# Kernel tuning notes

Hardware: AMD Instinct MI355X
Metric: run time of the kernel (lower is better)

## Reference

```python
import jax, jax.numpy as jnp
import numpy as np
import math

B, T = 512, 512
ENC = 512          # 2 * input_size
N_MELS, R = 80, 2
ATTN, DEC = 256, 256
PRE_H, PRE_O = 256, 256
HID = 128          # DCA hidden
SC, SK = 8, 21     # static channels / kernel
DC, DK = 8, 21     # dynamic channels / kernel
PL, PA, PB = 11, 0.1, 0.9  # prior length, alpha, beta


def _betabinom_pmf(k, n, a, b):
    lg = math.lgamma
    return math.exp(lg(n + 1) - lg(k + 1) - lg(n - k + 1)
                    + lg(k + a) + lg(n - k + b) - lg(n + a + b)
                    - (lg(a) + lg(b) - lg(a + b)))


def setup_inputs() -> dict:
    key = jax.random.key(0)
    ks = iter(jax.random.split(key, 64))
    def rn(shape, s=0.05):
        return jax.random.normal(next(ks), shape, dtype=jnp.float32) * s
    inp = {}
    inp["h"] = rn([B, T, ENC], 1.0)
    inp["y"] = rn([B, N_MELS], 1.0)
    a = jax.random.uniform(next(ks), [B, T], dtype=jnp.float32)
    inp["alpha"] = a / a.sum(-1, keepdims=True)  # valid attention distribution
    inp["c"] = rn([B, ENC], 1.0)
    for n in ["attn_h0", "attn_c0", "rnn1_h0", "rnn1_c0", "rnn2_h0", "rnn2_c0"]:
        inp[n] = rn([B, ATTN], 1.0)
    # prenet
    inp["fc1_w"] = rn([PRE_H, N_MELS]); inp["fc1_b"] = rn([PRE_H])
    inp["fc2_w"] = rn([PRE_O, PRE_H]); inp["fc2_b"] = rn([PRE_O])
    # dynamic convolution attention
    inp["W_w"] = rn([HID, ATTN]); inp["W_b"] = rn([HID])
    inp["V_w"] = rn([DC * DK, HID])
    inp["F_w"] = rn([SC, 1, SK])
    inp["U_w"] = rn([HID, SC])
    inp["T_w"] = rn([HID, DC]); inp["T_b"] = rn([HID])
    inp["v_w"] = rn([1, HID])
    P = np.array([_betabinom_pmf(k, PL - 1, PA, PB) for k in range(PL)], np.float32)[::-1].copy()
    inp["P"] = jnp.asarray(P)
    # attn LSTM cell: input = 2*input_size + prenet output = 768
    inp["attn_wih"] = rn([4 * ATTN, ENC + PRE_O]); inp["attn_whh"] = rn([4 * ATTN, ATTN])
    inp["attn_bih"] = rn([4 * ATTN]); inp["attn_bhh"] = rn([4 * ATTN])
    inp["lin_w"] = rn([DEC, ENC + ATTN]); inp["lin_b"] = rn([DEC])
    for pfx in ["r1", "r2"]:
        inp[pfx + "_wih"] = rn([4 * DEC, DEC]); inp[pfx + "_whh"] = rn([4 * DEC, DEC])
        inp[pfx + "_bih"] = rn([4 * DEC]); inp[pfx + "_bhh"] = rn([4 * DEC])
    inp["proj_w"] = rn([N_MELS * R, DEC])
    return inp


def _lstm(x, h, c, wih, whh, bih, bhh):
    g = x @ wih.T + bih + h @ whh.T + bhh
    i, f, gg, o = jnp.split(g, 4, axis=-1)
    c2 = jax.nn.sigmoid(f) * c + jax.nn.sigmoid(i) * jnp.tanh(gg)
    return jax.nn.sigmoid(o) * jnp.tanh(c2), c2


def _win(x, k):
    # x: [B, T + k - 1] padded signal -> sliding windows [B, T, k]
    idx = jnp.arange(T)[:, None] + jnp.arange(k)[None, :]
    return x[:, idx]


def reference(h, y, alpha, c, attn_h0, attn_c0, rnn1_h0, rnn1_c0, rnn2_h0, rnn2_c0,
              fc1_w, fc1_b, fc2_w, fc2_b, W_w, W_b, V_w, F_w, U_w, T_w, T_b, v_w, P,
              attn_wih, attn_whh, attn_bih, attn_bhh, lin_w, lin_b,
              r1_wih, r1_whh, r1_bih, r1_bhh, r2_wih, r2_whh, r2_bih, r2_bhh, proj_w):
    # prenet (eval mode -> dropout inactive since fixed=False)
    yp = jax.nn.relu(jax.nn.relu(y @ fc1_w.T + fc1_b) @ fc2_w.T + fc2_b)
    attn_h, attn_c = _lstm(jnp.concatenate([c, yp], -1), attn_h0, attn_c0,
                           attn_wih, attn_whh, attn_bih, attn_bhh)
    # --- dynamic convolution attention ---
    # prior: causal conv with flipped beta-binomial pmf
    p = jnp.einsum('btk,k->bt', _win(jnp.pad(alpha, ((0, 0), (PL - 1, 0))), PL), P)
    p = jnp.log(jnp.clip(p, 1e-6))
    # dynamic filters per batch element: [B, DC, DK]
    G = (jnp.tanh(attn_h @ W_w.T + W_b) @ V_w.T).reshape(-1, DC, DK)
    wd = _win(jnp.pad(alpha, ((0, 0), ((DK - 1) // 2, (DK - 1) // 2))), DK)  # [B,T,DK]
    g = jnp.einsum('btk,bck->btc', wd, G)  # grouped conv1d, groups=B
    ws = _win(jnp.pad(alpha, ((0, 0), ((SK - 1) // 2, (SK - 1) // 2))), SK)
    f = jnp.einsum('btk,ck->btc', ws, F_w[:, 0, :])  # static conv1d
    e = jnp.squeeze(jnp.tanh(f @ U_w.T + g @ T_w.T + T_b) @ v_w.T, -1) + p
    alpha2 = jax.nn.softmax(e, axis=-1)
    # --- context + decoder stack ---
    c2 = jnp.einsum('bt,btd->bd', alpha2, h)
    x = jnp.concatenate([c2, attn_h], -1) @ lin_w.T + lin_b
    r1_h, r1_c = _lstm(x, rnn1_h0, rnn1_c0, r1_wih, r1_whh, r1_bih, r1_bhh)
    x = x + r1_h
    r2_h, r2_c = _lstm(x, rnn2_h0, rnn2_c0, r2_wih, r2_whh, r2_bih, r2_bhh)
    x = x + r2_h
    out = (x @ proj_w.T).reshape(-1, N_MELS, R)
    return (out, alpha2, c2, attn_h, attn_c, r1_h, r1_c, r2_h, r2_c)
```

## Files before the change

### kernel.cpp

```cpp
#include <hip/hip_runtime.h>

typedef unsigned short u16;

__device__ __forceinline__ float bf2f(u16 u) { return __uint_as_float(((unsigned)u) << 16); }
__device__ __forceinline__ float ldraw(const void* p, size_t i, int dt) {
    return dt ? ((const float*)p)[i] : bf2f(((const u16*)p)[i]);
}
__device__ __forceinline__ int fl(const int* F, int f) { return f < 0 ? 1 : F[f]; }
__device__ __forceinline__ float fast_tanh(float x) {
    x = fminf(fmaxf(x, -15.f), 15.f);
    float e = __expf(2.f * x);
    return (e - 1.f) / (e + 1.f);
}
__device__ __forceinline__ float sigm(float x) { return 1.f / (1.f + __expf(-x)); }

__global__ __launch_bounds__(256) void k_detect(int* __restrict__ flagsRaw,
    const void* p0, const void* p1, const void* p2, const void* p3, const void* p4,
    const void* p5, const void* p6, const void* p7, const void* p8, const void* p9,
    const void* p10, const void* p11, const void* p12, const void* p13, const void* p14,
    const void* p15, const void* p16, const void* p17, const void* p18, const void* p19,
    const void* p20, const void* p21, const void* p22, const void* p23, const void* p24,
    const void* p25, const void* p26, const void* p27, const void* p28, const void* p29,
    const void* p30, const void* p31, const void* p32, const void* p33, const void* p34,
    const void* p35, const void* p36, const void* p37)
{
    const void* ptrs[38] = {p0,p1,p2,p3,p4,p5,p6,p7,p8,p9,p10,p11,p12,p13,p14,p15,p16,
                            p17,p18,p19,p20,p21,p22,p23,p24,p25,p26,p27,p28,p29,p30,p31,
                            p32,p33,p34,p35,p36,p37};
    const int ns[38] = {134217728, 40960, 262144, 262144,
                        131072,131072,131072,131072,131072,131072,
                        20480,256,65536,256,
                        32768,128,21504,168,1024,1024,128,128,11,
                        786432,262144,1024,1024, 196608,256,
                        262144,262144,1024,1024, 262144,262144,1024,1024, 40960};
    __shared__ int s;
    int b = blockIdx.x, tid = threadIdx.x;
    if (tid == 0) s = 0;
    __syncthreads();
    int nsamp = ns[b] >> 1;
    if (nsamp > 512) nsamp = 512;
    const u16* q = (const u16*)ptrs[b];
    int bad = 0;
    for (int i = tid; i < nsamp; i += 256) {
        u16 u = q[2 * i];
        int e = (u >> 7) & 0xff;
        bad += (e < 96 || e > 159) ? 1 : 0;
    }
    atomicAdd(&s, bad);
    __syncthreads();
    if (tid == 0) flagsRaw[b] = (s * 4 > nsamp) ? 1 : 0;
}

__global__ __launch_bounds__(256) void k_finish(
    const int* __restrict__ FRAW, int* __restrict__ FF,
    const void* U_w, const void* T_w, const void* T_b, const void* v_w, const void* F_w,
    float* utw, float* tbf, float* vf, float* ff)
{
    __shared__ int sflag[38];
    const int big[38] = {1,1,1,1, 1,1,1,1,1,1, 1,0,1,0,
                         1,0,1,0,1,1,0,0,0, 1,1,1,1, 1,0,
                         1,1,1,1, 1,1,1,1, 1};
    int tid = threadIdx.x;
    if (tid == 0) {
        int s = 0, c = 0;
        for (int i = 0; i < 38; i++) if (big[i]) { s += FRAW[i]; c++; }
        int maj = (s * 2 > c) ? 1 : 0;
        for (int i = 0; i < 38; i++) { int v = big[i] ? FRAW[i] : maj; sflag[i] = v; FF[i] = v; }
    }
    __syncthreads();
    int dU = sflag[18], dT = sflag[19], dTb = sflag[20], dV = sflag[21], dF = sflag[17];
    for (int i = tid; i < 1024; i += 256) {
        int j = i >> 3, c = i & 7;
        utw[j * 16 + c]     = ldraw(U_w, i, dU);
        utw[j * 16 + 8 + c] = ldraw(T_w, i, dT);
    }
    if (tid < 128) { tbf[tid] = ldraw(T_b, tid, dTb); vf[tid] = ldraw(v_w, tid, dV); }
    if (tid < 168) ff[tid] = ldraw(F_w, tid, dF);
}

__device__ __forceinline__ void vg32_pair(const int* F,
    const void* A, int lda, int fa, const void* B, int ldb, int bo, int fb, int K,
    int m0, int n0, int N, int tid, int tx, int ty, float* acc,
    float As[32][68], float Bs[32][68])
{
    int dA = fl(F, fa), dB = fl(F, fb);
    bool fastp = dA && dB;
    for (int k0 = 0; k0 < K; k0 += 64) {
        __syncthreads();
        if (fastp) {
            #pragma unroll
            for (int p = 0; p < 2; p++) {
                int e = tid + p * 256;
                int row = e >> 4, kk = (e & 15) * 4;
                float4 va = {0.f, 0.f, 0.f, 0.f};
                if (k0 + kk < K)
                    va = *(const float4*)((const float*)A + (size_t)(m0 + row) * lda + k0 + kk);
                *(float4*)&As[row][kk] = va;
                int nr = n0 + row;
                float4 vb = {0.f, 0.f, 0.f, 0.f};
                if (nr < N && k0 + kk < K)
                    vb = *(const float4*)((const float*)B + (size_t)nr * ldb + bo + k0 + kk);
                *(float4*)&Bs[row][kk] = vb;
            }
        } else {
            #pragma unroll
            for (int p = 0; p < 8; p++) {
                int e = tid + p * 256;
                int row = e >> 6, kk = e & 63;
                As[row][kk] = (k0 + kk < K) ? ldraw(A, (size_t)(m0 + row) * lda + k0 + kk, dA) : 0.f;
                int nr = n0 + row;
                Bs[row][kk] = (nr < N && k0 + kk < K)
                            ? ldraw(B, (size_t)nr * ldb + bo + k0 + kk, dB) : 0.f;
            }
        }
        __syncthreads();
        #pragma unroll
        for (int kq = 0; kq < 16; kq++) {
            float4 a0 = *(const float4*)&As[ty][kq * 4];
            float4 a1 = *(const float4*)&As[ty + 16][kq * 4];
            float4 b0 = *(const float4*)&Bs[tx][kq * 4];
            float4 b1 = *(const float4*)&Bs[tx + 16][kq * 4];
            acc[0] += a0.x*b0.x + a0.y*b0.y + a0.z*b0.z + a0.w*b0.w;
            acc[1] += a0.x*b1.x + a0.y*b1.y + a0.z*b1.z + a0.w*b1.w;
            acc[2] += a1.x*b0.x + a1.y*b0.y + a1.z*b0.z + a1.w*b0.w;
            acc[3] += a1.x*b1.x + a1.y*b1.y + a1.z*b1.z + a1.w*b1.w;
        }
    }
}

__global__ __launch_bounds__(256) void k_vgemm32(
    const int* __restrict__ F,
    const void* A1, int lda1, int fa1, const void* B1, int ldb1, int bo1, int fb1, int K1,
    const void* A2, int lda2, int fa2, const void* B2, int ldb2, int bo2, int fb2, int K2,
    const void* A3, int lda3, int fa3, const void* B3, int ldb3, int bo3, int fb3, int K3,
    const void* bias1, int fx1, const void* bias2, int fx2,
    float* __restrict__ Cf, int ldc, int N, int act)
{
    __shared__ float As[32][68], Bs[32][68];
    int tid = threadIdx.x, tx = tid & 15, ty = tid >> 4;
    int m0 = blockIdx.y * 32, n0 = blockIdx.x * 32;
    float acc[4] = {0.f, 0.f, 0.f, 0.f};
    vg32_pair(F, A1, lda1, fa1, B1, ldb1, bo1, fb1, K1, m0, n0, N, tid, tx, ty, acc, As, Bs);
    if (A2) vg32_pair(F, A2, lda2, fa2, B2, ldb2, bo2, fb2, K2, m0, n0, N, tid, tx, ty, acc, As, Bs);
    if (A3) vg32_pair(F, A3, lda3, fa3, B3, ldb3, bo3, fb3, K3, m0, n0, N, tid, tx, ty, acc, As, Bs);

    #pragma unroll
    for (int c = 0; c < 2; c++) {
        int n = n0 + tx + c * 16;
        if (n >= N) continue;
        float bias = 0.f;
        if (bias1) bias += ldraw(bias1, n, fl(F, fx1));
        if (bias2) bias += ldraw(bias2, n, fl(F, fx2));
        #pragma unroll
        for (int r = 0; r < 2; r++) {
            float v = acc[r * 2 + c] + bias;
            if (act == 1) v = fmaxf(v, 0.f);
            else if (act == 2) v = fast_tanh(v);
            Cf[(size_t)(m0 + ty + r * 16) * ldc + n] = v;
        }
    }
}

__device__ __forceinline__ void lstm_pair(const int* F,
    const void* A, int lda, int fa, const void* B, int ldb, int bo, int fb, int K,
    int b0, int j0, int tid, int tx, int ty, float* acc,
    float As[16][68], float Bs[64][68])
{
    int dA = fl(F, fa), dB = fl(F, fb);
    bool fastp = dA && dB;
    for (int k0 = 0; k0 < K; k0 += 64) {
        __syncthreads();
        if (fastp) {
            {
                int e = tid;
                int row = e >> 4, kk = (e & 15) * 4;
                float4 va = {0.f, 0.f, 0.f, 0.f};
                if (k0 + kk < K)
                    va = *(const float4*)((const float*)A + (size_t)(b0 + row) * lda + k0 + kk);
                *(float4*)&As[row][kk] = va;
            }
            #pragma unroll
            for (int p = 0; p < 4; p++) {
                int e = tid + p * 256;
                int brow = e >> 4, kk = (e & 15) * 4;
                int grow = (brow >> 4) * 256 + j0 + (brow & 15);
                float4 vb = {0.f, 0.f, 0.f, 0.f};
                if (k0 + kk < K)
                    vb = *(const float4*)((const float*)B + (size_t)grow * ldb + bo + k0 + kk);
                *(float4*)&Bs[brow][kk] = vb;
            }
        } else {
            #pragma unroll
            for (int p = 0; p < 4; p++) {
                int e = tid + p * 256;
                int row = e >> 6, kk = e & 63;
                As[row][kk] = (k0 + kk < K) ? ldraw(A, (size_t)(b0 + row) * lda + k0 + kk, dA) : 0.f;
            }
            #pragma unroll
            for (int p = 0; p < 16; p++) {
                int e = tid + p * 256;
                int brow = e >> 6, kk = e & 63;
                int grow = (brow >> 4) * 256 + j0 + (brow & 15);
                Bs[brow][kk] = (k0 + kk < K)
                             ? ldraw(B, (size_t)grow * ldb + bo + k0 + kk, dB) : 0.f;
            }
        }
        __syncthreads();
        #pragma unroll
        for (int kq = 0; kq < 16; kq++) {
            float4 a = *(const float4*)&As[ty][kq * 4];
            #pragma unroll
            for (int g = 0; g < 4; g++) {
                float4 b = *(const float4*)&Bs[g * 16 + tx][kq * 4];
                acc[g] += a.x*b.x + a.y*b.y + a.z*b.z + a.w*b.w;
            }
        }
    }
}

__global__ __launch_bounds__(256) void k_lstm(
    const int* __restrict__ F,
    const void* A1, int lda1, int fa1, const void* B1, int ldb1, int bo1, int fb1, int K1,
    const void* A2, int lda2, int fa2, const void* B2, int ldb2, int bo2, int fb2, int K2,
    const void* A3, int lda3, int fa3, const void* B3, int ldb3, int bo3, int fb3, int K3,
    const void* bih, int fx1, const void* bhh, int fx2,
    const void* c0, int fc0,
    float* __restrict__ h_out, float* __restrict__ c_out,
    const float* __restrict__ xprev, float* __restrict__ xout)
{
    __shared__ float As[16][68];
    __shared__ float Bs[64][68];
    int tid = threadIdx.x, tx = tid & 15, ty = tid >> 4;
    int j0 = blockIdx.x * 16, b0 = blockIdx.y * 16;
    float acc[4] = {0.f, 0.f, 0.f, 0.f};
    lstm_pair(F, A1, lda1, fa1, B1, ldb1, bo1, fb1, K1, b0, j0, tid, tx, ty, acc, As, Bs);
    if (A2) lstm_pair(F, A2, lda2, fa2, B2, ldb2, bo2, fb2, K2, b0, j0, tid, tx, ty, acc, As, Bs);
    if (A3) lstm_pair(F, A3, lda3, fa3, B3, ldb3, bo3, fb3, K3, b0, j0, tid, tx, ty, acc, As, Bs);

    int j = j0 + tx, b = b0 + ty;
    int dx1 = fl(F, fx1), dx2 = fl(F, fx2);
    float gi = acc[0] + ldraw(bih, j, dx1)       + ldraw(bhh, j, dx2);
    float gf = acc[1] + ldraw(bih, j + 256, dx1) + ldraw(bhh, j + 256, dx2);
    float gg = acc[2] + ldraw(bih, j + 512, dx1) + ldraw(bhh, j + 512, dx2);
    float go = acc[3] + ldraw(bih, j + 768, dx1) + ldraw(bhh, j + 768, dx2);
    size_t idx = (size_t)b * 256 + j;
    float cp = ldraw(c0, idx, F[fc0]);
    float cn = sigm(gf) * cp + sigm(gi) * fast_tanh(gg);
    float hn = sigm(go) * fast_tanh(cn);
    h_out[idx] = hn;
    c_out[idx] = cn;
    if (xprev) xout[idx] = xprev[idx] + hn;
}

__global__ __launch_bounds__(256) void k_dca(
    const int* __restrict__ F, const void* __restrict__ alpha, const void* __restrict__ P,
    const float* __restrict__ G, const float* __restrict__ utw, const float* __restrict__ tbf,
    const float* __restrict__ vf, const float* __restrict__ ff,
    float* __restrict__ o_a2)
{
    __shared__ float4 sut[512];
    __shared__ float stb[128], sv[128], sff[168], sgd[168], sal[532], spf[16], sred[8];
    int dA = F[2], dP = F[22];
    int b = blockIdx.x, tid = threadIdx.x;
    for (int i = tid; i < 512; i += 256) sut[i] = ((const float4*)utw)[i];
    if (tid < 128) { stb[tid] = tbf[tid]; sv[tid] = vf[tid]; }
    if (tid < 168) { sff[tid] = ff[tid]; sgd[tid] = G[(size_t)b * 168 + tid]; }
    if (tid < 11)  spf[tid] = ldraw(P, tid, dP);
    for (int i = tid; i < 532; i += 256)
        sal[i] = (i >= 10 && i < 522) ? ldraw(alpha, (size_t)b * 512 + i - 10, dA) : 0.f;
    __syncthreads();

    float e[2];
    #pragma unroll
    for (int q = 0; q < 2; q++) {
        int t = tid + q * 256;
        float aw[21];
        #pragma unroll
        for (int k = 0; k < 21; k++) aw[k] = sal[t + k];
        float pv = 0.f;
        #pragma unroll
        for (int k = 0; k < 11; k++) pv += aw[k] * spf[k];
        float fc[8], gc[8];
        #pragma unroll
        for (int c = 0; c < 8; c++) {
            float s1 = 0.f, s2 = 0.f;
            #pragma unroll
            for (int k = 0; k < 21; k++) {
                s1 += aw[k] * sff[c * 21 + k];
                s2 += aw[k] * sgd[c * 21 + k];
            }
            fc[c] = s1; gc[c] = s2;
        }
        float ev = 0.f;
        #pragma unroll 4
        for (int j = 0; j < 128; j++) {
            float4 u0 = sut[j * 4 + 0], u1 = sut[j * 4 + 1];
            float4 t0 = sut[j * 4 + 2], t1 = sut[j * 4 + 3];
            float a = stb[j];
            a += fc[0] * u0.x + fc[1] * u0.y + fc[2] * u0.z + fc[3] * u0.w;
            a += fc[4] * u1.x + fc[5] * u1.y + fc[6] * u1.z + fc[7] * u1.w;
            a += gc[0] * t0.x + gc[1] * t0.y + gc[2] * t0.z + gc[3] * t0.w;
            a += gc[4] * t1.x + gc[5] * t1.y + gc[6] * t1.z + gc[7] * t1.w;
            ev += fast_tanh(a) * sv[j];
        }
        e[q] = ev + __logf(fmaxf(pv, 1e-6f));
    }

    float m = fmaxf(e[0], e[1]);
    #pragma unroll
    for (int off = 32; off >= 1; off >>= 1) m = fmaxf(m, __shfl_xor(m, off));
    if ((tid & 63) == 0) sred[tid >> 6] = m;
    __syncthreads();
    m = fmaxf(fmaxf(sred[0], sred[1]), fmaxf(sred[2], sred[3]));
    float x0 = __expf(e[0] - m), x1 = __expf(e[1] - m);
    float s = x0 + x1;
    #pragma unroll
    for (int off = 32; off >= 1; off >>= 1) s += __shfl_xor(s, off);
    if ((tid & 63) == 0) sred[4 + (tid >> 6)] = s;
    __syncthreads();
    s = sred[4] + sred[5] + sred[6] + sred[7];
    float inv = 1.f / s;
    o_a2[(size_t)b * 512 + tid]       = x0 * inv;
    o_a2[(size_t)b * 512 + tid + 256] = x1 * inv;
}

__global__ __launch_bounds__(256) void k_c2_part(
    const int* __restrict__ F, const float* __restrict__ a2,
    const void* __restrict__ h, float* __restrict__ part)
{
    int dH = F[0];
    int bi = blockIdx.x;
    int b = bi >> 1, sp = bi & 1;
    int tid = threadIdx.x;
    int dsub = (tid & 63) * 8;
    int tsub = tid >> 6;
    __shared__ float sa[256];
    sa[tid] = a2[(size_t)b * 512 + sp * 256 + tid];
    __syncthreads();
    float acc[8];
    #pragma unroll
    for (int j = 0; j < 8; j++) acc[j] = 0.f;
    size_t rowbase = (size_t)b * 512 + sp * 256;
    if (dH) {
        const float* hf = (const float*)h;
        for (int tt = tsub; tt < 256; tt += 4) {
            float a = sa[tt];
            const float* p = hf + (rowbase + tt) * 512 + dsub;
            float4 v0 = *(const float4*)p, v1 = *(const float4*)(p + 4);
            acc[0] += a * v0.x; acc[1] += a * v0.y; acc[2] += a * v0.z; acc[3] += a * v0.w;
            acc[4] += a * v1.x; acc[5] += a * v1.y; acc[6] += a * v1.z; acc[7] += a * v1.w;
        }
    } else {
        const u16* hb = (const u16*)h;
        for (int tt = tsub; tt < 256; tt += 4) {
            float a = sa[tt];
            const u16* p = hb + (rowbase + tt) * 512 + dsub;
            #pragma unroll
            for (int j = 0; j < 8; j++) acc[j] += a * bf2f(p[j]);
        }
    }
    __shared__ float sacc[256 * 8];
    #pragma unroll
    for (int j = 0; j < 8; j++) sacc[tid * 8 + j] = acc[j];
    __syncthreads();
    if (tid < 64) {
        float* pp = part + ((size_t)sp * 512 + b) * 512 + tid * 8;
        #pragma unroll
        for (int j = 0; j < 8; j++)
            pp[j] = sacc[tid * 8 + j] + sacc[(tid + 64) * 8 + j]
                  + sacc[(tid + 128) * 8 + j] + sacc[(tid + 192) * 8 + j];
    }
}

__global__ void k_c2_red(const float* __restrict__ part, float* __restrict__ o_c2)
{
    int idx = blockIdx.x * 256 + threadIdx.x;
    o_c2[idx] = part[idx] + part[idx + 262144];
}

__global__ void k_plant_direct(float* out0, float v) {
    if (threadIdx.x == 0 && blockIdx.x == 0) out0[0] = v;
}

extern "C" void kernel_launch(void* const* d_in, const int* in_sizes, int n_in,
                              void* d_out, int out_size, void* d_ws, size_t ws_size,
                              hipStream_t stream)
{
    (void)out_size; (void)ws_size;
    float* outf = (float*)d_out;

    static const int exp_sizes[38] = {
        134217728, 40960, 262144, 262144,
        131072,131072,131072,131072,131072,131072,
        20480,256,65536,256,
        32768,128,21504,168,1024,1024,128,128,11,
        786432,262144,1024,1024, 196608,256,
        262144,262144,1024,1024, 262144,262144,1024,1024, 40960};
    int bad = 0;
    if (n_in != 38) bad = 100;
    else for (int i = 0; i < 38; i++)
        if (in_sizes[i] != exp_sizes[i]) { bad = i + 1; break; }
    if (bad) {
        k_plant_direct<<<1, 1, 0, stream>>>(outf, 4194304.f + 65536.f * (float)bad);
        return;
    }

    const void* h_enc  = d_in[0];  const void* y      = d_in[1];
    const void* alpha  = d_in[2];  const void* c_in   = d_in[3];
    const void* ah0    = d_in[4];  const void* ac0    = d_in[5];
    const void* r1h0   = d_in[6];  const void* r1c0   = d_in[7];
    const void* r2h0   = d_in[8];  const void* r2c0   = d_in[9];
    const void* fc1_w  = d_in[10]; const void* fc1_b  = d_in[11];
    const void* fc2_w  = d_in[12]; const void* fc2_b  = d_in[13];
    const void* W_w    = d_in[14]; const void* W_b    = d_in[15];
    const void* V_w    = d_in[16]; const void* F_w    = d_in[17];
    const void* U_w    = d_in[18]; const void* T_w    = d_in[19];
    const void* T_b    = d_in[20]; const void* v_w    = d_in[21];
    const void* P      = d_in[22];
    const void* a_wih  = d_in[23]; const void* a_whh  = d_in[24];
    const void* a_bih  = d_in[25]; const void* a_bhh  = d_in[26];
    const void* lin_w  = d_in[27]; const void* lin_b  = d_in[28];
    const void* r1_wih = d_in[29]; const void* r1_whh = d_in[30];
    const void* r1_bih = d_in[31]; const void* r1_bhh = d_in[32];
    const void* r2_wih = d_in[33]; const void* r2_whh = d_in[34];
    const void* r2_bih = d_in[35]; const void* r2_bhh = d_in[36];
    const void* proj_w = d_in[37];

    char* ws = (char*)d_ws;
    int*   FRAW = (int*)  (ws + 0);
    int*   FF   = (int*)  (ws + 256);
    float* utw  = (float*)(ws + 1024);
    float* tbf  = (float*)(ws + 9216);
    float* vf   = (float*)(ws + 9728);
    float* ffs  = (float*)(ws + 10240);
    float* h1f  = (float*)(ws + 12288);
    float* ypf  = (float*)(ws + 536576);
    float* thf  = (float*)(ws + 1060864);
    float* Gdf  = (float*)(ws + 1323008);
    float* part = (float*)(ws + 1667072);

    float* o_out = outf + 0;
    float* o_a2  = outf + 81920;
    float* o_c2  = outf + 344064;
    float* o_ah  = outf + 606208;
    float* o_ac  = outf + 737280;
    float* o_r1h = outf + 868352;
    float* o_r1c = outf + 999424;
    float* o_r2h = outf + 1130496;
    float* o_r2c = outf + 1261568;

    const void* nv = nullptr;
    dim3 blk(256, 1, 1);

    k_detect<<<38, blk, 0, stream>>>(FRAW,
        d_in[0], d_in[1], d_in[2], d_in[3], d_in[4], d_in[5], d_in[6], d_in[7], d_in[8],
        d_in[9], d_in[10], d_in[11], d_in[12], d_in[13], d_in[14], d_in[15], d_in[16],
        d_in[17], d_in[18], d_in[19], d_in[20], d_in[21], d_in[22], d_in[23], d_in[24],
        d_in[25], d_in[26], d_in[27], d_in[28], d_in[29], d_in[30], d_in[31], d_in[32],
        d_in[33], d_in[34], d_in[35], d_in[36], d_in[37]);
    k_finish<<<1, blk, 0, stream>>>(FRAW, FF, U_w, T_w, T_b, v_w, F_w, utw, tbf, vf, ffs);

    k_vgemm32<<<dim3(8, 16), blk, 0, stream>>>(FF,
        y, 80, 1, fc1_w, 80, 0, 10, 80,
        nv, 0, -1, nv, 0, 0, -1, 0,  nv, 0, -1, nv, 0, 0, -1, 0,
        fc1_b, 11, nv, -1, h1f, 256, 256, 1);
    k_vgemm32<<<dim3(8, 16), blk, 0, stream>>>(FF,
        h1f, 256, -1, fc2_w, 256, 0, 12, 256,
        nv, 0, -1, nv, 0, 0, -1, 0,  nv, 0, -1, nv, 0, 0, -1, 0,
        fc2_b, 13, nv, -1, ypf, 256, 256, 1);

    k_lstm<<<dim3(16, 32), blk, 0, stream>>>(FF,
        c_in, 512, 3, a_wih, 768, 0, 23, 512,
        ypf, 256, -1, a_wih, 768, 512, 23, 256,
        ah0, 256, 4, a_whh, 256, 0, 24, 256,
        a_bih, 25, a_bhh, 26, ac0, 5, o_ah, o_ac, nullptr, nullptr);

    k_vgemm32<<<dim3(4, 16), blk, 0, stream>>>(FF,
        o_ah, 256, -1, W_w, 256, 0, 14, 256,
        nv, 0, -1, nv, 0, 0, -1, 0,  nv, 0, -1, nv, 0, 0, -1, 0,
        W_b, 15, nv, -1, thf, 128, 128, 2);
    k_vgemm32<<<dim3(6, 16), blk, 0, stream>>>(FF,
        thf, 128, -1, V_w, 128, 0, 16, 128,
        nv, 0, -1, nv, 0, 0, -1, 0,  nv, 0, -1, nv, 0, 0, -1, 0,
        nv, -1, nv, -1, Gdf, 168, 168, 0);

    k_dca<<<512, blk, 0, stream>>>(FF, alpha, P, Gdf, utw, tbf, vf, ffs, o_a2);

    k_c2_part<<<1024, blk, 0, stream>>>(FF, o_a2, h_enc, part);
    k_c2_red<<<1024, blk, 0, stream>>>(part, o_c2);

    float* x1f = h1f;
    float* x2f = ypf;
    k_vgemm32<<<dim3(8, 16), blk, 0, stream>>>(FF,
        o_c2, 512, -1, lin_w, 768, 0, 27, 512,
        o_ah, 256, -1, lin_w, 768, 512, 27, 256,
        nv, 0, -1, nv, 0, 0, -1, 0,
        lin_b, 28, nv, -1, x1f, 256, 256, 0);

    k_lstm<<<dim3(16, 32), blk, 0, stream>>>(FF,
        x1f, 256, -1, r1_wih, 256, 0, 29, 256,
        r1h0, 256, 6, r1_whh, 256, 0, 30, 256,
        nv, 0, -1, nv, 0, 0, -1, 0,
        r1_bih, 31, r1_bhh, 32, r1c0, 7, o_r1h, o_r1c, x1f, x2f);

    float* x3f = h1f;
    k_lstm<<<dim3(16, 32), blk, 0, stream>>>(FF,
        x2f, 256, -1, r2_wih, 256, 0, 33, 256,
        r2h0, 256, 8, r2_whh, 256, 0, 34, 256,
        nv, 0, -1, nv, 0, 0, -1, 0,
        r2_bih, 35, r2_bhh, 36, r2c0, 9, o_r2h, o_r2c, x2f, x3f);

    k_vgemm32<<<dim3(5, 16), blk, 0, stream>>>(FF,
        x3f, 256, -1, proj_w, 256, 0, 37, 256,
        nv, 0, -1, nv, 0, 0, -1, 0,  nv, 0, -1, nv, 0, 0, -1, 0,
        nv, -1, nv, -1, o_out, 160, 160, 0);
}
```

Before: 359.0 us.

## Use bf16 MFMA for LSTM gate GEMMs with smem gate exchange

Replaces the scalar fp32 FMA inner product in the LSTM kernel with bf16 MFMA 16x16x32 instructions. Each of the four waves computes one gate tile, and fp32 inputs are converted to bf16 while staged into shared memory. The accumulators are written to shared memory so the elementwise LSTM update can gather all four gates. This lowers matmul instruction cost but reduces input precision to bf16 and drops the K-boundary guards.

```diff
diff --git a/kernel.cpp b/kernel.cpp
--- a/kernel.cpp
+++ b/kernel.cpp
@@ -1,8 +1,14 @@
 #include <hip/hip_runtime.h>
 
 typedef unsigned short u16;
+typedef __attribute__((ext_vector_type(8))) short s8v;
+typedef __attribute__((ext_vector_type(4))) float f32x4;
 
 __device__ __forceinline__ float bf2f(u16 u) { return __uint_as_float(((unsigned)u) << 16); }
+__device__ __forceinline__ u16 f2bf(float f) {
+    unsigned u = __float_as_uint(f);
+    return (u16)((u + 0x7fffu + ((u >> 16) & 1u)) >> 16);
+}
 __device__ __forceinline__ float ldraw(const void* p, size_t i, int dt) {
     return dt ? ((const float*)p)[i] : bf2f(((const u16*)p)[i]);
 }
@@ -161,60 +167,49 @@
     }
 }
 
-__device__ __forceinline__ void lstm_pair(const int* F,
+__device__ __forceinline__ void lstm_mfma_piece(const int* F,
     const void* A, int lda, int fa, const void* B, int ldb, int bo, int fb, int K,
-    int b0, int j0, int tid, int tx, int ty, float* acc,
-    float As[16][68], float Bs[64][68])
+    int b0, int j0, int tid, int wave, int lane, f32x4& acc,
+    u16 As[16][72], u16 Bs[64][72])
 {
     int dA = fl(F, fa), dB = fl(F, fb);
-    bool fastp = dA && dB;
     for (int k0 = 0; k0 < K; k0 += 64) {
         __syncthreads();
-        if (fastp) {
-            {
-                int e = tid;
-                int row = e >> 4, kk = (e & 15) * 4;
-                float4 va = {0.f, 0.f, 0.f, 0.f};
-                if (k0 + kk < K)
-                    va = *(const float4*)((const float*)A + (size_t)(b0 + row) * lda + k0 + kk);
-                *(float4*)&As[row][kk] = va;
+        for (int g = tid; g < 640; g += 256) {
+            const void* src; int dt; size_t idx; u16* dst;
+            if (g < 128) {
+                int row = g >> 3, kg = (g & 7) * 8;
+                idx = (size_t)(b0 + row) * lda + k0 + kg;
+                src = A; dt = dA; dst = &As[row][kg];
+            } else {
+                int gb = g - 128;
+                int row = gb >> 3, kg = (gb & 7) * 8;
+                int grow = (row >> 4) * 256 + j0 + (row & 15);
+                idx = (size_t)grow * ldb + bo + k0 + kg;
+                src = B; dt = dB; dst = &Bs[row][kg];
             }
-            #pragma unroll
-            for (int p = 0; p < 4; p++) {
-                int e = tid + p * 256;
-                int brow = e >> 4, kk = (e & 15) * 4;
-                int grow = (brow >> 4) * 256 + j0 + (brow & 15);
-                float4 vb = {0.f, 0.f, 0.f, 0.f};
-                if (k0 + kk < K)
-                    vb = *(const float4*)((const float*)B + (size_t)grow * ldb + bo + k0 + kk);
-                *(float4*)&Bs[brow][kk] = vb;
+            if (dt) {
+                const float* sp = (const float*)src + idx;
+                float4 a = *(const float4*)sp;
+                float4 b = *(const float4*)(sp + 4);
+                s8v v;
+                v[0] = (short)f2bf(a.x); v[1] = (short)f2bf(a.y);
+                v[2] = (short)f2bf(a.z); v[3] = (short)f2bf(a.w);
+                v[4] = (short)f2bf(b.x); v[5] = (short)f2bf(b.y);
+                v[6] = (short)f2bf(b.z); v[7] = (short)f2bf(b.w);
+                *(s8v*)dst = v;
+            } else {
+                *(s8v*)dst = *(const s8v*)((const u16*)src + idx);
             }
-        } else {
-            #pragma unroll
-            for (int p = 0; p < 4; p++) {
-                int e = tid + p * 256;
-                int row = e >> 6, kk = e & 63;
-                As[row][kk] = (k0 + kk < K) ? ldraw(A, (size_t)(b0 + row) * lda + k0 + kk, dA) : 0.f;
-            }
-            #pragma unroll
-            for (int p = 0; p < 16; p++) {
-                int e = tid + p * 256;
-                int brow = e >> 6, kk = e & 63;
-                int grow = (brow >> 4) * 256 + j0 + (brow & 15);
-                Bs[brow][kk] = (k0 + kk < K)
-                             ? ldraw(B, (size_t)grow * ldb + bo + k0 + kk, dB) : 0.f;
-            }
         }
         __syncthreads();
-        #pragma unroll
-        for (int kq = 0; kq < 16; kq++) {
-            float4 a = *(const float4*)&As[ty][kq * 4];
-            #pragma unroll
-            for (int g = 0; g < 4; g++) {
-                float4 b = *(const float4*)&Bs[g * 16 + tx][kq * 4];
-                acc[g] += a.x*b.x + a.y*b.y + a.z*b.z + a.w*b.w;
-            }
-        }
+        int r = lane & 15, kg = (lane >> 4) * 8;
+        s8v a0 = *(const s8v*)&As[r][kg];
+        s8v w0 = *(const s8v*)&Bs[wave * 16 + r][kg];
+        acc = __builtin_amdgcn_mfma_f32_16x16x32_bf16(a0, w0, acc, 0, 0, 0);
+        s8v a1 = *(const s8v*)&As[r][32 + kg];
+        s8v w1 = *(const s8v*)&Bs[wave * 16 + r][32 + kg];
+        acc = __builtin_amdgcn_mfma_f32_16x16x32_bf16(a1, w1, acc, 0, 0, 0);
     }
 }
 
@@ -228,21 +223,28 @@
     float* __restrict__ h_out, float* __restrict__ c_out,
     const float* __restrict__ xprev, float* __restrict__ xout)
 {
-    __shared__ float As[16][68];
-    __shared__ float Bs[64][68];
-    int tid = threadIdx.x, tx = tid & 15, ty = tid >> 4;
+    __shared__ u16 As[16][72];
+    __shared__ u16 Bs[64][72];
+    __shared__ float sG[4][16][16];
+    int tid = threadIdx.x, lane = tid & 63, wave = tid >> 6;
     int j0 = blockIdx.x * 16, b0 = blockIdx.y * 16;
-    float acc[4] = {0.f, 0.f, 0.f, 0.f};
-    lstm_pair(F, A1, lda1, fa1, B1, ldb1, bo1, fb1, K1, b0, j0, tid, tx, ty, acc, As, Bs);
-    if (A2) lstm_pair(F, A2, lda2, fa2, B2, ldb2, bo2, fb2, K2, b0, j0, tid, tx, ty, acc, As, Bs);
-    if (A3) lstm_pair(F, A3, lda3, fa3, B3, ldb3, bo3, fb3, K3, b0, j0, tid, tx, ty, acc, As, Bs);
-
-    int j = j0 + tx, b = b0 + ty;
+    f32x4 acc = {0.f, 0.f, 0.f, 0.f};
+    lstm_mfma_piece(F, A1, lda1, fa1, B1, ldb1, bo1, fb1, K1, b0, j0, tid, wave, lane, acc, As, Bs);
+    if (A2) lstm_mfma_piece(F, A2, lda2, fa2, B2, ldb2, bo2, fb2, K2, b0, j0, tid, wave, lane, acc, As, Bs);
+    if (A3) lstm_mfma_piece(F, A3, lda3, fa3, B3, ldb3, bo3, fb3, K3, b0, j0, tid, wave, lane, acc, As, Bs);
+
+    #pragma unroll
+    for (int r2 = 0; r2 < 4; r2++)
+        sG[wave][(lane >> 4) * 4 + r2][lane & 15] = acc[r2];
+    __syncthreads();
+
+    int jl = tid & 15, bl = tid >> 4;
+    int j = j0 + jl, b = b0 + bl;
     int dx1 = fl(F, fx1), dx2 = fl(F, fx2);
-    float gi = acc[0] + ldraw(bih, j, dx1)       + ldraw(bhh, j, dx2);
-    float gf = acc[1] + ldraw(bih, j + 256, dx1) + ldraw(bhh, j + 256, dx2);
-    float gg = acc[2] + ldraw(bih, j + 512, dx1) + ldraw(bhh, j + 512, dx2);
-    float go = acc[3] + ldraw(bih, j + 768, dx1) + ldraw(bhh, j + 768, dx2);
+    float gi = sG[0][bl][jl] + ldraw(bih, j, dx1)       + ldraw(bhh, j, dx2);
+    float gf = sG[1][bl][jl] + ldraw(bih, j + 256, dx1) + ldraw(bhh, j + 256, dx2);
+    float gg = sG[2][bl][jl] + ldraw(bih, j + 512, dx1) + ldraw(bhh, j + 512, dx2);
+    float go = sG[3][bl][jl] + ldraw(bih, j + 768, dx1) + ldraw(bhh, j + 768, dx2);
     size_t idx = (size_t)b * 256 + j;
     float cp = ldraw(c0, idx, F[fc0]);
     float cn = sigm(gf) * cp + sigm(gi) * fast_tanh(gg);
```

Result: faster. 337.7 us (-5.9%).
